# Kernel optimization log

Measured on AMD Instinct MI355X. Metric: run time of the kernel, lower is better.

Reference implementation:

```python
import jax, jax.numpy as jnp
import numpy as np

BITWIDTH = 7
M, K, N = 32768, 1024, 1024  # tokens, in_features, out_features


def _clip8(x):
    return jnp.clip(x, -127, 127).astype(jnp.int8)


def _range_bits(x):
    # RangeEstimate: ceil(log2(max|x|)) as int, 0 if all-zero
    r = jnp.max(jnp.abs(x).astype(jnp.float32))
    bits = jnp.ceil(jnp.log2(jnp.maximum(r, 1.0)))
    return jnp.where(r == 0, 0, bits).astype(jnp.int32)


def _round_shift(x, shift):
    # RoundShift (stochastic-style bit-shift rounding); shift is a traced int32 >= 1
    p = jnp.left_shift(jnp.int32(1), shift)
    rt = jnp.floor_divide(x, p)
    prob = x - rt * p
    dec = jnp.floor_divide(prob, jnp.left_shift(jnp.int32(1), shift - 1))
    return _clip8(rt + dec)


def setup_inputs() -> dict:
    key = jax.random.key(0)
    k1, k2 = jax.random.split(key)
    act_in = jax.random.randint(k1, (M, K), -127, 128, dtype=jnp.int32).astype(jnp.int8)
    weight = jax.random.randint(k2, (N, K), -127, 128, dtype=jnp.int32).astype(jnp.int8)
    exp_in = jnp.int32(0)
    weight_exp = jnp.int32(-11)  # ceil(log2(xavier bound)) - 7 for 1024x1024
    return {"act_in": act_in, "weight": weight, "exp_in": exp_in, "weight_exp": weight_exp}


def reference(act_in, weight, exp_in, weight_exp):
    # int8 GEMM with int32 accumulation: [M,K] @ [K,N]
    acc = jnp.matmul(act_in.astype(jnp.int32), weight.T.astype(jnp.int32))
    # act_calc: range-estimate + conditional bit-shift requantize to int8
    bits = _range_bits(acc)
    shift = bits - BITWIDTH
    pos = shift > 0
    sc = jnp.maximum(shift, 1)  # safe shift for the untaken branch
    act_out = jnp.where(pos, _round_shift(acc, sc), acc.astype(jnp.int8))
    exp_out = jnp.where(pos, exp_in + weight_exp + shift, exp_in + weight_exp)
    return act_out, exp_out
```

## Files before the change

kernel.cpp:

```cpp
#include <hip/hip_runtime.h>
#include <stdint.h>


#define MM 32768
#define NN 1024
#define KK 1024
#define BM 256
#define BN 128
#define BK 128
#define NKT (KK / BK)
#define TILE_A (BM * BK)
#define TILE_B (BN * BK)

typedef __attribute__((ext_vector_type(4))) int i32x4;
typedef __attribute__((ext_vector_type(16))) int i32x16;

__device__ __forceinline__ int pack4(int a, int b, int c, int d) {
  return (int)((unsigned)(a & 0xff) | ((unsigned)(b & 0xff) << 8) |
               ((unsigned)(c & 0xff) << 16) | ((unsigned)(d & 0xff) << 24));
}

__global__ void k_init(unsigned* slot) {
  if (threadIdx.x == 0) *slot = 0u;
}

__global__ void k_pack(const int* __restrict__ src, int8_t* __restrict__ dst, int n) {
  long t = (long)blockIdx.x * blockDim.x + threadIdx.x;
  long stride = (long)gridDim.x * blockDim.x;
  for (long i = t * 16; i < (long)n; i += stride * 16) {
    const i32x4* s = (const i32x4*)(src + i);
    i32x4 a0 = s[0], a1 = s[1], a2 = s[2], a3 = s[3];
    i32x4 o;
    o[0] = pack4(a0[0], a0[1], a0[2], a0[3]);
    o[1] = pack4(a1[0], a1[1], a1[2], a1[3]);
    o[2] = pack4(a2[0], a2[1], a2[2], a2[3]);
    o[3] = pack4(a3[0], a3[1], a3[2], a3[3]);
    *(i32x4*)(dst + i) = o;
  }
}

__global__ __launch_bounds__(512, 2)
void k_gemm(const int8_t* __restrict__ A8, const int8_t* __restrict__ B8,
            int* __restrict__ out, unsigned* __restrict__ maxslot) {
  __shared__ int8_t As[3][TILE_A];
  __shared__ int8_t Bs[3][TILE_B];

  const int tid  = threadIdx.x;
  const int lane = tid & 63;
  const int w    = tid >> 6;
  const int wm   = w >> 1;
  const int wn   = w & 1;

  const int orig = blockIdx.x;
  const int wgid = ((orig & 7) << 7) + (orig >> 3);
  const int bn = wgid & 7;
  const int bm = wgid >> 3;
  const int m0 = bm * BM;
  const int n0 = bn * BN;

  i32x16 acc[2][2];
#pragma unroll
  for (int i = 0; i < 2; ++i)
#pragma unroll
    for (int j = 0; j < 2; ++j) acc[i][j] = 0;

  auto stageA = [&](int buf, int kt, int L) {
    const int p   = w * 4096 + L * 1024 + lane * 16;
    const int row = p >> 7;
    const int col = (p & 127) ^ ((row & 7) << 4);
    __builtin_amdgcn_global_load_lds(
        (const __attribute__((address_space(1))) void*)(A8 + (size_t)(m0 + row) * KK + kt * BK + col),
        (__attribute__((address_space(3))) void*)(&As[buf][w * 4096 + L * 1024]),
        16, 0, 0);
  };
  auto stageB = [&](int buf, int kt, int L) {
    const int p   = w * 2048 + L * 1024 + lane * 16;
    const int row = p >> 7;
    const int col = (p & 127) ^ ((row & 7) << 4);
    __builtin_amdgcn_global_load_lds(
        (const __attribute__((address_space(1))) void*)(B8 + (size_t)(n0 + row) * KK + kt * BK + col),
        (__attribute__((address_space(3))) void*)(&Bs[buf][w * 2048 + L * 1024]),
        16, 0, 0);
  };

  stageA(0, 0, 0); stageA(0, 0, 1); stageA(0, 0, 2); stageA(0, 0, 3);
  stageB(0, 0, 0); stageB(0, 0, 1);
  stageA(1, 1, 0); stageA(1, 1, 1); stageA(1, 1, 2); stageA(1, 1, 3);
  stageB(1, 1, 0); stageB(1, 1, 1);
  asm volatile("s_waitcnt vmcnt(6)" ::: "memory");
  __builtin_amdgcn_sched_barrier(0);
  __builtin_amdgcn_s_barrier();

  int cur = 0;
  for (int kt = 0; kt < NKT; ++kt) {
    int nxt = cur + 2; if (nxt >= 3) nxt -= 3;
    const bool more = (kt + 2 < NKT);
#pragma unroll
    for (int q = 0; q < 2; ++q) {
      if (more) {
        if (q == 0) { stageA(nxt, kt + 2, 0); stageA(nxt, kt + 2, 1); stageB(nxt, kt + 2, 0); }
        else        { stageA(nxt, kt + 2, 2); stageA(nxt, kt + 2, 3); stageB(nxt, kt + 2, 1); }
      }
      i32x4 af[2][4], bf[4];
#pragma unroll
      for (int ks = 0; ks < 4; ++ks) {
        const int brow = wn * 64 + q * 32 + (lane & 31);
        const int ba = brow * BK + ((ks * 32 + ((lane >> 5) << 4)) ^ ((brow & 7) << 4));
        bf[ks] = *(const i32x4*)(&Bs[cur][ba]);
      }
#pragma unroll
      for (int mi = 0; mi < 2; ++mi)
#pragma unroll
        for (int ks = 0; ks < 4; ++ks) {
          const int arow = wm * 64 + mi * 32 + (lane & 31);
          const int aa = arow * BK + ((ks * 32 + ((lane >> 5) << 4)) ^ ((arow & 7) << 4));
          af[mi][ks] = *(const i32x4*)(&As[cur][aa]);
        }
      __builtin_amdgcn_sched_barrier(0);
      __builtin_amdgcn_s_barrier();
      __builtin_amdgcn_s_setprio(1);
#pragma unroll
      for (int ks = 0; ks < 4; ++ks)
#pragma unroll
        for (int mi = 0; mi < 2; ++mi)
          acc[mi][q] = __builtin_amdgcn_mfma_i32_32x32x32_i8(
              af[mi][ks], bf[ks], acc[mi][q], 0, 0, 0);
      __builtin_amdgcn_s_setprio(0);
      if (q == 1) {
        if (more)                 { asm volatile("s_waitcnt vmcnt(6)" ::: "memory"); }
        else if (kt + 1 < NKT)    { asm volatile("s_waitcnt vmcnt(0)" ::: "memory"); }
      }
      __builtin_amdgcn_sched_barrier(0);
      __builtin_amdgcn_s_barrier();
    }
    cur = cur + 1 == 3 ? 0 : cur + 1;
  }

  int mx = 0;
#pragma unroll
  for (int mi = 0; mi < 2; ++mi)
#pragma unroll
    for (int ni = 0; ni < 2; ++ni)
#pragma unroll
      for (int rg = 0; rg < 16; ++rg) {
        int x = acc[mi][ni][rg];
        int a = x < 0 ? -x : x;
        mx = a > mx ? a : mx;
      }
#pragma unroll
  for (int off = 32; off >= 1; off >>= 1) {
    int o = __shfl_xor(mx, off);
    mx = o > mx ? o : mx;
  }
  if (lane == 0) atomicMax(maxslot, (unsigned)mx);

#pragma unroll
  for (int mi = 0; mi < 2; ++mi)
#pragma unroll
    for (int ni = 0; ni < 2; ++ni) {
      const int mbase = m0 + wm * 64 + mi * 32;
      const int ncol  = n0 + wn * 64 + ni * 32 + (lane & 31);
#pragma unroll
      for (int rg = 0; rg < 16; ++rg) {
        const int mrow = mbase + (rg & 3) + ((rg >> 2) << 3) + ((lane >> 5) << 2);
        out[(size_t)mrow * NN + ncol] = acc[mi][ni][rg];
      }
    }
}

__global__ __launch_bounds__(256, 2)
void k_gemm_fb(const int* __restrict__ A32, const int* __restrict__ B32,
               int* __restrict__ out, unsigned* __restrict__ maxslot) {
  __shared__ int8_t As[128 * 128];
  __shared__ int8_t Bs[128 * 128];
  const int tid = threadIdx.x, lane = tid & 63, w = tid >> 6;
  const int wr = w >> 1, wc = w & 1;
  const int bn = blockIdx.x & 7, bm = blockIdx.x >> 3;
  const int m0 = bm * 128, n0 = bn * 128;
  i32x16 acc[2][2];
#pragma unroll
  for (int i = 0; i < 2; ++i)
#pragma unroll
    for (int j = 0; j < 2; ++j) acc[i][j] = 0;
  for (int kt = 0; kt < 8; ++kt) {
    const int k0 = kt * 128;
    __syncthreads();
#pragma unroll
    for (int j = 0; j < 4; ++j) {
      const int fb = (j * 256 + tid) * 16;
      const int row = fb >> 7;
      const int swz = fb ^ ((row & 7) << 4);
      const int col = fb & 127;
      const int* sa = A32 + (size_t)(m0 + row) * KK + k0 + col;
      const int* sb = B32 + (size_t)(n0 + row) * KK + k0 + col;
      i32x4 av, bv;
#pragma unroll
      for (int t = 0; t < 4; ++t) {
        i32x4 ta = ((const i32x4*)sa)[t];
        i32x4 tb = ((const i32x4*)sb)[t];
        av[t] = pack4(ta[0], ta[1], ta[2], ta[3]);
        bv[t] = pack4(tb[0], tb[1], tb[2], tb[3]);
      }
      *(i32x4*)(As + swz) = av;
      *(i32x4*)(Bs + swz) = bv;
    }
    __syncthreads();
#pragma unroll
    for (int ks = 0; ks < 4; ++ks) {
      i32x4 af[2], bf[2];
#pragma unroll
      for (int mi = 0; mi < 2; ++mi) {
        const int row = wr * 64 + mi * 32 + (lane & 31);
        int a = row * 128 + ks * 32 + ((lane >> 5) << 4);
        a ^= (row & 7) << 4;
        af[mi] = *(const i32x4*)(As + a);
      }
#pragma unroll
      for (int ni = 0; ni < 2; ++ni) {
        const int row = wc * 64 + ni * 32 + (lane & 31);
        int a = row * 128 + ks * 32 + ((lane >> 5) << 4);
        a ^= (row & 7) << 4;
        bf[ni] = *(const i32x4*)(Bs + a);
      }
#pragma unroll
      for (int mi = 0; mi < 2; ++mi)
#pragma unroll
        for (int ni = 0; ni < 2; ++ni)
          acc[mi][ni] = __builtin_amdgcn_mfma_i32_32x32x32_i8(
              af[mi], bf[ni], acc[mi][ni], 0, 0, 0);
    }
  }
  int mx = 0;
#pragma unroll
  for (int mi = 0; mi < 2; ++mi)
#pragma unroll
    for (int ni = 0; ni < 2; ++ni)
#pragma unroll
      for (int rg = 0; rg < 16; ++rg) {
        int x = acc[mi][ni][rg];
        int a = x < 0 ? -x : x;
        mx = a > mx ? a : mx;
      }
#pragma unroll
  for (int off = 32; off >= 1; off >>= 1) {
    int o = __shfl_xor(mx, off);
    mx = o > mx ? o : mx;
  }
  if (lane == 0) atomicMax(maxslot, (unsigned)mx);
#pragma unroll
  for (int mi = 0; mi < 2; ++mi)
#pragma unroll
    for (int ni = 0; ni < 2; ++ni) {
      const int mbase = m0 + wr * 64 + mi * 32;
      const int ncol = n0 + wc * 64 + ni * 32 + (lane & 31);
#pragma unroll
      for (int rg = 0; rg < 16; ++rg) {
        const int mrow = mbase + (rg & 3) + ((rg >> 2) << 3) + ((lane >> 5) << 2);
        out[(size_t)mrow * NN + ncol] = acc[mi][ni][rg];
      }
    }
}

__global__ __launch_bounds__(256)
void k_requant(int* __restrict__ out, const unsigned* __restrict__ maxslot) {
  const unsigned r = *maxslot;
  const int bits  = (r <= 1u) ? 0 : (32 - __clz((int)(r - 1u)));
  const int shift = bits - 7;
  const size_t n = (size_t)MM * NN;
  size_t i = ((size_t)blockIdx.x * blockDim.x + threadIdx.x) * 4;
  const size_t stride = (size_t)gridDim.x * blockDim.x * 4;
  if (shift > 0) {
    for (; i < n; i += stride) {
      i32x4 v = *(i32x4*)(out + i);
#pragma unroll
      for (int j = 0; j < 4; ++j) {
        const int x = v[j];
        int t = (x >> shift) + ((x >> (shift - 1)) & 1);
        v[j] = t > 127 ? 127 : (t < -127 ? -127 : t);
      }
      *(i32x4*)(out + i) = v;
    }
  } else {
    for (; i < n; i += stride) {
      i32x4 v = *(i32x4*)(out + i);
#pragma unroll
      for (int j = 0; j < 4; ++j) v[j] = (int)(int8_t)v[j];
      *(i32x4*)(out + i) = v;
    }
  }
}

__global__ void k_final(int* __restrict__ out, const int* __restrict__ exp_in,
                        const int* __restrict__ wexp) {
  if (threadIdx.x == 0) {
    const unsigned r = *(const unsigned*)(out + (size_t)MM * NN);
    const int bits  = (r <= 1u) ? 0 : (32 - __clz((int)(r - 1u)));
    const int shift = bits - 7;
    out[(size_t)MM * NN] = *exp_in + *wexp + (shift > 0 ? shift : 0);
  }
}

extern "C" void kernel_launch(void* const* d_in, const int* in_sizes, int n_in,
                              void* d_out, int out_size, void* d_ws, size_t ws_size,
                              hipStream_t stream) {
  const int* act    = (const int*)d_in[0];
  const int* wgt    = (const int*)d_in[1];
  const int* exp_in = (const int*)d_in[2];
  const int* wexp   = (const int*)d_in[3];
  int* out          = (int*)d_out;
  unsigned* maxslot = (unsigned*)(out + (size_t)MM * NN);

  const size_t need = (size_t)(MM + NN) * KK + 256;

  k_init<<<1, 64, 0, stream>>>(maxslot);

  if (ws_size >= need) {
    int8_t* a8 = (int8_t*)d_ws;
    int8_t* w8 = a8 + (size_t)MM * KK;
    k_pack<<<2048, 256, 0, stream>>>(act, a8, MM * KK);
    k_pack<<<256, 256, 0, stream>>>(wgt, w8, NN * KK);
    const int grid = (MM / BM) * (NN / BN);
    k_gemm<<<grid, 512, 0, stream>>>(a8, w8, out, maxslot);
  } else {
    k_gemm_fb<<<(MM / 128) * (NN / 128), 256, 0, stream>>>(act, wgt, out, maxslot);
  }

  k_requant<<<4096, 256, 0, stream>>>(out, maxslot);
  k_final<<<1, 64, 0, stream>>>(out, exp_in, wexp);
}
```

Measured before the change: 211.9 us.

## Retile int8 GEMM to 256x256x64 with double-buffered LDS and simpler sync

Grows the block tile from 256x128 to 256x256 and shrinks K-step from 128 to 64, raising arithmetic intensity per block. The triple-buffered pipeline with explicit vmcnt waits and split barriers is replaced by a double-buffered loop with one __syncthreads per k-step, and the LDS swizzle pattern changes to fit 64-byte rows. Each wave now owns a 128x64 output tile with 8 accumulators, which raises register pressure, and launch_bounds asks for 4 blocks per CU. The simpler sync may expose global-load latency that the previous schedule hid.

Measured after the change: 785.2 us. 270% more time.

```diff
diff --git a/kernel.cpp b/kernel.cpp
--- a/kernel.cpp
+++ b/kernel.cpp
@@ -6,11 +6,9 @@
 #define NN 1024
 #define KK 1024
 #define BM 256
-#define BN 128
-#define BK 128
+#define BN 256
+#define BK 64
 #define NKT (KK / BK)
-#define TILE_A (BM * BK)
-#define TILE_B (BN * BK)
 
 typedef __attribute__((ext_vector_type(4))) int i32x4;
 typedef __attribute__((ext_vector_type(16))) int i32x16;
@@ -39,106 +37,89 @@
   }
 }
 
-__global__ __launch_bounds__(512, 2)
+__global__ __launch_bounds__(512, 4)
 void k_gemm(const int8_t* __restrict__ A8, const int8_t* __restrict__ B8,
             int* __restrict__ out, unsigned* __restrict__ maxslot) {
-  __shared__ int8_t As[3][TILE_A];
-  __shared__ int8_t Bs[3][TILE_B];
+  __shared__ int8_t As[2][BM * BK];
+  __shared__ int8_t Bs[2][BN * BK];
 
   const int tid  = threadIdx.x;
   const int lane = tid & 63;
   const int w    = tid >> 6;
-  const int wm   = w >> 1;
-  const int wn   = w & 1;
+  const int wm   = w >> 2;
+  const int wn   = w & 3;
 
   const int orig = blockIdx.x;
-  const int wgid = ((orig & 7) << 7) + (orig >> 3);
-  const int bn = wgid & 7;
-  const int bm = wgid >> 3;
+  const int wgid = ((orig & 7) << 6) + (orig >> 3);
+  const int bn = wgid & 3;
+  const int bm = wgid >> 2;
   const int m0 = bm * BM;
   const int n0 = bn * BN;
 
-  i32x16 acc[2][2];
-#pragma unroll
-  for (int i = 0; i < 2; ++i)
+  i32x16 acc[4][2];
+#pragma unroll
+  for (int i = 0; i < 4; ++i)
 #pragma unroll
     for (int j = 0; j < 2; ++j) acc[i][j] = 0;
 
-  auto stageA = [&](int buf, int kt, int L) {
-    const int p   = w * 4096 + L * 1024 + lane * 16;
-    const int row = p >> 7;
-    const int col = (p & 127) ^ ((row & 7) << 4);
-    __builtin_amdgcn_global_load_lds(
-        (const __attribute__((address_space(1))) void*)(A8 + (size_t)(m0 + row) * KK + kt * BK + col),
-        (__attribute__((address_space(3))) void*)(&As[buf][w * 4096 + L * 1024]),
-        16, 0, 0);
+  auto stage = [&](int buf, int kt) {
+    const int k0 = kt * BK;
+#pragma unroll
+    for (int q = 0; q < 2; ++q) {
+      const int p   = (w * 2 + q) * 1024 + lane * 16;
+      const int row = p >> 6;
+      const int col = (p & 63) ^ (((row >> 1) & 3) << 4);
+      __builtin_amdgcn_global_load_lds(
+          (const __attribute__((address_space(1))) void*)(A8 + (size_t)(m0 + row) * KK + k0 + col),
+          (__attribute__((address_space(3))) void*)(&As[buf][(w * 2 + q) * 1024]),
+          16, 0, 0);
+      __builtin_amdgcn_global_load_lds(
+          (const __attribute__((address_space(1))) void*)(B8 + (size_t)(n0 + row) * KK + k0 + col),
+          (__attribute__((address_space(3))) void*)(&Bs[buf][(w * 2 + q) * 1024]),
+          16, 0, 0);
+    }
   };
-  auto stageB = [&](int buf, int kt, int L) {
-    const int p   = w * 2048 + L * 1024 + lane * 16;
-    const int row = p >> 7;
-    const int col = (p & 127) ^ ((row & 7) << 4);
-    __builtin_amdgcn_global_load_lds(
-        (const __attribute__((address_space(1))) void*)(B8 + (size_t)(n0 + row) * KK + kt * BK + col),
-        (__attribute__((address_space(3))) void*)(&Bs[buf][w * 2048 + L * 1024]),
-        16, 0, 0);
+
+  auto compute = [&](int buf) {
+#pragma unroll
+    for (int ks = 0; ks < 2; ++ks) {
+      i32x4 af[4], bf[2];
+#pragma unroll
+      for (int ni = 0; ni < 2; ++ni) {
+        const int row = wn * 64 + ni * 32 + (lane & 31);
+        const int a = row * BK +
+            ((ks * 32 + ((lane >> 5) << 4)) ^ (((row >> 1) & 3) << 4));
+        bf[ni] = *(const i32x4*)(&Bs[buf][a]);
+      }
+#pragma unroll
+      for (int mi = 0; mi < 4; ++mi) {
+        const int row = wm * 128 + mi * 32 + (lane & 31);
+        const int a = row * BK +
+            ((ks * 32 + ((lane >> 5) << 4)) ^ (((row >> 1) & 3) << 4));
+        af[mi] = *(const i32x4*)(&As[buf][a]);
+      }
+      __builtin_amdgcn_s_setprio(1);
+#pragma unroll
+      for (int mi = 0; mi < 4; ++mi)
+#pragma unroll
+        for (int ni = 0; ni < 2; ++ni)
+          acc[mi][ni] = __builtin_amdgcn_mfma_i32_32x32x32_i8(
+              af[mi], bf[ni], acc[mi][ni], 0, 0, 0);
+      __builtin_amdgcn_s_setprio(0);
+    }
   };
 
-  stageA(0, 0, 0); stageA(0, 0, 1); stageA(0, 0, 2); stageA(0, 0, 3);
-  stageB(0, 0, 0); stageB(0, 0, 1);
-  stageA(1, 1, 0); stageA(1, 1, 1); stageA(1, 1, 2); stageA(1, 1, 3);
-  stageB(1, 1, 0); stageB(1, 1, 1);
-  asm volatile("s_waitcnt vmcnt(6)" ::: "memory");
-  __builtin_amdgcn_sched_barrier(0);
-  __builtin_amdgcn_s_barrier();
-
-  int cur = 0;
+  stage(0, 0);
+  __syncthreads();
   for (int kt = 0; kt < NKT; ++kt) {
-    int nxt = cur + 2; if (nxt >= 3) nxt -= 3;
-    const bool more = (kt + 2 < NKT);
-#pragma unroll
-    for (int q = 0; q < 2; ++q) {
-      if (more) {
-        if (q == 0) { stageA(nxt, kt + 2, 0); stageA(nxt, kt + 2, 1); stageB(nxt, kt + 2, 0); }
-        else        { stageA(nxt, kt + 2, 2); stageA(nxt, kt + 2, 3); stageB(nxt, kt + 2, 1); }
-      }
-      i32x4 af[2][4], bf[4];
-#pragma unroll
-      for (int ks = 0; ks < 4; ++ks) {
-        const int brow = wn * 64 + q * 32 + (lane & 31);
-        const int ba = brow * BK + ((ks * 32 + ((lane >> 5) << 4)) ^ ((brow & 7) << 4));
-        bf[ks] = *(const i32x4*)(&Bs[cur][ba]);
-      }
-#pragma unroll
-      for (int mi = 0; mi < 2; ++mi)
-#pragma unroll
-        for (int ks = 0; ks < 4; ++ks) {
-          const int arow = wm * 64 + mi * 32 + (lane & 31);
-          const int aa = arow * BK + ((ks * 32 + ((lane >> 5) << 4)) ^ ((arow & 7) << 4));
-          af[mi][ks] = *(const i32x4*)(&As[cur][aa]);
-        }
-      __builtin_amdgcn_sched_barrier(0);
-      __builtin_amdgcn_s_barrier();
-      __builtin_amdgcn_s_setprio(1);
-#pragma unroll
-      for (int ks = 0; ks < 4; ++ks)
-#pragma unroll
-        for (int mi = 0; mi < 2; ++mi)
-          acc[mi][q] = __builtin_amdgcn_mfma_i32_32x32x32_i8(
-              af[mi][ks], bf[ks], acc[mi][q], 0, 0, 0);
-      __builtin_amdgcn_s_setprio(0);
-      if (q == 1) {
-        if (more)                 { asm volatile("s_waitcnt vmcnt(6)" ::: "memory"); }
-        else if (kt + 1 < NKT)    { asm volatile("s_waitcnt vmcnt(0)" ::: "memory"); }
-      }
-      __builtin_amdgcn_sched_barrier(0);
-      __builtin_amdgcn_s_barrier();
-    }
-    cur = cur + 1 == 3 ? 0 : cur + 1;
+    if (kt + 1 < NKT) stage((kt + 1) & 1, kt + 1);
+    compute(kt & 1);
+    __syncthreads();
   }
 
   int mx = 0;
 #pragma unroll
-  for (int mi = 0; mi < 2; ++mi)
+  for (int mi = 0; mi < 4; ++mi)
 #pragma unroll
     for (int ni = 0; ni < 2; ++ni)
 #pragma unroll
@@ -155,10 +136,10 @@
   if (lane == 0) atomicMax(maxslot, (unsigned)mx);
 
 #pragma unroll
-  for (int mi = 0; mi < 2; ++mi)
+  for (int mi = 0; mi < 4; ++mi)
 #pragma unroll
     for (int ni = 0; ni < 2; ++ni) {
-      const int mbase = m0 + wm * 64 + mi * 32;
+      const int mbase = m0 + wm * 128 + mi * 32;
       const int ncol  = n0 + wn * 64 + ni * 32 + (lane & 31);
 #pragma unroll
       for (int rg = 0; rg < 16; ++rg) {
```
